# Kernel tuning notes

Hardware: AMD Instinct MI355X
Metric: run time of the kernel (lower is better)

## Reference

```python
import jax, jax.numpy as jnp
import numpy as np

N_EMBD = 1024
N_HEAD = 16

def setup_inputs() -> dict:
    key = jax.random.key(0)
    ks = jax.random.split(key, 5)
    s = 0.02
    return {
        "x": jax.random.normal(ks[0], (4, 2048, N_EMBD), dtype=jnp.float32),
        "w_attn": jax.random.normal(ks[1], (N_EMBD, 3 * N_EMBD), dtype=jnp.float32) * s,
        "b_attn": jnp.zeros((3 * N_EMBD,), dtype=jnp.float32),
        "w_proj": jax.random.normal(ks[2], (N_EMBD, N_EMBD), dtype=jnp.float32) * s,
        "b_proj": jnp.zeros((N_EMBD,), dtype=jnp.float32),
    }

def reference(x, w_attn, b_attn, w_proj, b_proj):
    B, T, C = x.shape
    H = N_HEAD
    D = C // H
    qkv = x @ w_attn + b_attn                       # [B,T,3C]
    q, k, v = jnp.split(qkv, 3, axis=-1)
    # [B,H,T,D]
    q = q.reshape(B, T, H, D).transpose(0, 2, 1, 3)
    k = k.reshape(B, T, H, D).transpose(0, 2, 1, 3)
    v = v.reshape(B, T, H, D).transpose(0, 2, 1, 3)
    scale = 1.0 / jnp.sqrt(jnp.asarray(D, dtype=x.dtype))
    attn = jnp.einsum("bhqd,bhkd->bhqk", q, k) * scale
    mask = jnp.tril(jnp.ones((T, T), dtype=bool))
    attn = jnp.where(mask, attn, jnp.asarray(-jnp.inf, dtype=attn.dtype))
    attn = jax.nn.softmax(attn, axis=-1)
    out = jnp.einsum("bhqk,bhkd->bhqd", attn, v)    # [B,H,T,D]
    out = out.transpose(0, 2, 1, 3).reshape(B, T, C)
    return out @ w_proj + b_proj
```

## Files before the change

### kernel.cpp

```cpp
#include <hip/hip_runtime.h>


typedef unsigned short u16b;
typedef __bf16 bf16x8 __attribute__((ext_vector_type(8)));
typedef float f32x4 __attribute__((ext_vector_type(4)));
typedef float f32x16 __attribute__((ext_vector_type(16)));
typedef unsigned short u16x4 __attribute__((ext_vector_type(4)));

#define AS1(p) ((const __attribute__((address_space(1))) void*)(p))
#define AS3(p) ((__attribute__((address_space(3))) void*)(p))
#define GLDS(g, l) __builtin_amdgcn_global_load_lds(AS1(g), AS3(l), 16, 0, 0)

__device__ __forceinline__ u16b bfr(float v) {
  union { float f; unsigned u; } x; x.f = v;
  unsigned r = x.u + 0x7fffu + ((x.u >> 16) & 1u);
  return (u16b)(r >> 16);
}

__device__ __forceinline__ unsigned pk2(float lo, float hi) {
  union { __bf16 h[2]; unsigned u; } t;
  t.h[0] = (__bf16)lo; t.h[1] = (__bf16)hi;
  return t.u;
}

__global__ __launch_bounds__(256) void cvt_bf16_kernel(
    const float* __restrict__ src, u16b* __restrict__ dst, int n4) {
  int i = blockIdx.x * 256 + threadIdx.x;
  const int stride = gridDim.x * 256;
  for (; i < n4; i += stride) {
    const float4 v = reinterpret_cast<const float4*>(src)[i];
    u16x4 o;
    o[0] = bfr(v.x); o[1] = bfr(v.y); o[2] = bfr(v.z); o[3] = bfr(v.w);
    reinterpret_cast<u16x4*>(dst)[i] = o;
  }
}

__global__ __launch_bounds__(256) void transpose_cvt_kernel(
    const float* __restrict__ src, u16b* __restrict__ dst, int R, int C) {
  __shared__ u16b tile[64][72];
  const int nc = C >> 6;
  const int br = blockIdx.x / nc, bc = blockIdx.x % nc;
  const int r0 = br << 6, c0 = bc << 6;
  const int c = threadIdx.x & 63, r4 = threadIdx.x >> 6;
  #pragma unroll
  for (int i = 0; i < 16; ++i) {
    const int r = r4 + 4 * i;
    tile[r][c] = bfr(src[(size_t)(r0 + r) * C + c0 + c]);
  }
  __syncthreads();
  #pragma unroll
  for (int i = 0; i < 16; ++i) {
    const int rr = r4 + 4 * i;
    dst[(size_t)(c0 + rr) * R + r0 + c] = tile[c][rr];
  }
}

template <int EPI>
__global__ __launch_bounds__(256, 2) void gemm128_kernel(
    const u16b* __restrict__ A, const u16b* __restrict__ Bt,
    const float* __restrict__ bias,
    u16b* __restrict__ oQ, u16b* __restrict__ oK, u16b* __restrict__ oVt,
    float* __restrict__ oF, int M, int N, int K) {
  __shared__ u16b smem[32768];
  const int tid = threadIdx.x;
  const int wid = tid >> 6, lane = tid & 63;
  const int xcd = blockIdx.x & 7;
  const int idx = blockIdx.x >> 3;
  const int stg = idx >> 6, rr6 = idx & 63;
  const int brow = (xcd << 3) + (rr6 >> 3);
  const int bcol = (stg << 3) + (rr6 & 7);
  const int wr = (wid >> 1) << 6, wc = (wid & 1) << 6;

  f32x4 acc[4][4] = {};

  const int srow = (wid << 5) + (lane >> 3);
  const int sc = ((lane & 7) ^ (lane >> 3)) << 3;
  const u16b* Ab = A + (size_t)((brow << 7) + srow) * K + sc;
  const u16b* Bb = Bt + (size_t)((bcol << 7) + srow) * K + sc;
  const int fr = lane & 15;
  const int fq = lane >> 4;
  const int pcs0 = ((fq) ^ (fr & 7)) << 4;
  const int pcs1 = ((4 + fq) ^ (fr & 7)) << 4;
  const int nk = K >> 6;

#define STAGE(bufi, kk)                                                        \
  {                                                                            \
    char* sb = (char*)smem + (bufi) * 32768;                                   \
    _Pragma("unroll")                                                          \
    for (int j = 0; j < 4; ++j)                                                \
      GLDS(Ab + (size_t)8 * K * j + (kk), sb + wid * 4096 + j * 1024);         \
    _Pragma("unroll")                                                          \
    for (int j = 0; j < 4; ++j)                                                \
      GLDS(Bb + (size_t)8 * K * j + (kk), sb + 16384 + wid * 4096 + j * 1024); \
  }

  STAGE(0, 0);
  STAGE(1, 64);

  #pragma unroll 1
  for (int kt = 0; kt < nk; ++kt) {
    if (kt + 1 < nk) asm volatile("s_waitcnt vmcnt(8)" ::: "memory");
    else             asm volatile("s_waitcnt vmcnt(0)" ::: "memory");
    __builtin_amdgcn_s_barrier();

    const char* As = (const char*)smem + (kt & 1) * 32768;
    const char* Bs = As + 16384;
    bf16x8 af0[4], af1[4], bf0[4], bf1[4];
    #pragma unroll
    for (int i = 0; i < 4; ++i) {
      const int rowb = (wr + i * 16 + fr) * 128;
      af0[i] = *(const bf16x8*)(As + rowb + pcs0);
      af1[i] = *(const bf16x8*)(As + rowb + pcs1);
    }
    #pragma unroll
    for (int j = 0; j < 4; ++j) {
      const int rowb = (wc + j * 16 + fr) * 128;
      bf0[j] = *(const bf16x8*)(Bs + rowb + pcs0);
      bf1[j] = *(const bf16x8*)(Bs + rowb + pcs1);
    }
    __builtin_amdgcn_s_setprio(1);
    #pragma unroll
    for (int i = 0; i < 4; ++i)
      #pragma unroll
      for (int j = 0; j < 4; ++j)
        acc[i][j] = __builtin_amdgcn_mfma_f32_16x16x32_bf16(af0[i], bf0[j], acc[i][j], 0, 0, 0);
    #pragma unroll
    for (int i = 0; i < 4; ++i)
      #pragma unroll
      for (int j = 0; j < 4; ++j)
        acc[i][j] = __builtin_amdgcn_mfma_f32_16x16x32_bf16(af1[i], bf1[j], acc[i][j], 0, 0, 0);
    __builtin_amdgcn_s_setprio(0);

    __builtin_amdgcn_s_barrier();
    if (kt + 2 < nk) STAGE(kt & 1, (kt + 2) << 6);
  }
#undef STAGE

  if (EPI == 1) {
    #pragma unroll
    for (int j = 0; j < 4; ++j) {
      const int n0 = (bcol << 7) + wc + j * 16 + fr;
      const float bv = bias[n0];
      #pragma unroll
      for (int i = 0; i < 4; ++i) {
        #pragma unroll
        for (int r = 0; r < 4; ++r) {
          const int m0 = (brow << 7) + wr + i * 16 + fq * 4 + r;
          oF[(size_t)m0 * N + n0] = acc[i][j][r] + bv;
        }
      }
    }
  } else {
    const int sect = bcol >> 3;
    if (sect < 2) {
      const float qs = (sect == 0) ? 0.1803368801f : 1.0f;
      u16b* oPtr = (sect == 0) ? oQ : oK;
      u16b* tile = (u16b*)smem;
      #pragma unroll
      for (int j = 0; j < 4; ++j) {
        const int n = wc + j * 16 + fr;
        const float bv = bias[(bcol << 7) + n];
        #pragma unroll
        for (int i = 0; i < 4; ++i) {
          #pragma unroll
          for (int r = 0; r < 4; ++r) {
            const int m = wr + i * 16 + fq * 4 + r;
            const int byteoff = m * 256 + (((n >> 3) ^ (m & 7)) << 4) + ((n & 7) << 1);
            *(u16b*)((char*)tile + byteoff) = bfr((acc[i][j][r] + bv) * qs);
          }
        }
      }
      __syncthreads();
      const int nh = wid >> 1;
      const int c = lane & 7;
      #pragma unroll
      for (int it = 0; it < 8; ++it) {
        const int m = ((wid & 1) << 6) + (it << 3) + (lane >> 3);
        const int chunk = (nh << 3) + (c ^ (m & 7));
        const bf16x8 val = *(const bf16x8*)((const char*)tile + m * 256 + chunk * 16);
        const int m0 = (brow << 7) + m;
        const int n0 = (bcol << 7) + (nh << 6) + (c << 3);
        const int bb = m0 >> 11, tt = m0 & 2047;
        const int h = (n0 >> 6) & 15, d = n0 & 63;
        *(bf16x8*)(oPtr + (((size_t)(bb * 16 + h) * 2048 + tt) * 64 + d)) = val;
      }
    } else {
      u16b* tile = (u16b*)smem;
      #pragma unroll
      for (int j = 0; j < 4; ++j) {
        const int nl = wc + j * 16 + fr;
        const float bv = bias[(bcol << 7) + nl];
        #pragma unroll
        for (int i = 0; i < 4; ++i) {
          #pragma unroll
          for (int r = 0; r < 4; ++r) {
            const int m = wr + i * 16 + fq * 4 + r;
            const int byteoff = nl * 256 + (((m >> 3) ^ (nl & 7)) << 4) + ((m & 7) << 1);
            *(u16b*)((char*)tile + byteoff) = bfr(acc[i][j][r] + bv);
          }
        }
      }
      __syncthreads();
      const int row0 = wid << 5;
      const int c16 = lane & 15;
      const int rw = lane >> 4;
      const int t0 = (brow << 7) & 2047;
      const int bb = brow >> 4;
      #pragma unroll
      for (int it = 0; it < 8; ++it) {
        const int nl = row0 + (it << 2) + rw;
        const int pch = c16 ^ (nl & 7);
        const bf16x8 val = *(const bf16x8*)((const char*)tile + nl * 256 + pch * 16);
        const int h = ((bcol & 7) << 1) + (nl >> 6);
        const int d = nl & 63;
        *(bf16x8*)(oVt + ((size_t)((bb << 4) + h) * 64 + d) * 2048 + t0 + (c16 << 3)) = val;
      }
    }
  }
}

__global__ __launch_bounds__(256, 3) void flash_kernel(
    const u16b* __restrict__ Q, const u16b* __restrict__ K,
    const u16b* __restrict__ Vt, u16b* __restrict__ O) {
  __shared__ u16b smem[24576];
  const int bid = blockIdx.x;
  const int bh = bid & 63;
  const int qt = 15 - (bid >> 6);
  const int tid = threadIdx.x, wid = tid >> 6, lane = tid & 63;
  const int ln31 = lane & 31, hi = lane >> 5;
  const size_t baseQK = (size_t)bh * 2048 * 64;
  const size_t baseV = (size_t)bh * 64 * 2048;
  const int b = bh >> 4, h = bh & 15;
  const int srow = wid * 8 + (lane >> 3);
  const int sc = ((lane & 7) ^ (srow & 7)) << 3;

  const int q0w = (qt << 7) + wid * 32;
  const int NT = 2 * qt + 2;
  const int LT = q0w >> 6;

#define FSTAGE(kt, bi)                                                         \
  {                                                                            \
    char* kb_ = (char*)smem + (bi) * 16384;                                    \
    const int k0_ = (kt) << 6;                                                 \
    GLDS(K + baseQK + (size_t)(k0_ + srow) * 64 + sc,        kb_ + wid * 1024);\
    GLDS(K + baseQK + (size_t)(k0_ + 32 + srow) * 64 + sc,   kb_ + 4096 + wid * 1024);\
    GLDS(Vt + baseV + (size_t)srow * 2048 + k0_ + sc,        kb_ + 8192 + wid * 1024);\
    GLDS(Vt + baseV + (size_t)(32 + srow) * 2048 + k0_ + sc, kb_ + 12288 + wid * 1024);\
  }

  bf16x8 qf[4];
  {
    const u16b* qp = Q + baseQK + (size_t)(q0w + ln31) * 64 + hi * 8;
    #pragma unroll
    for (int kk = 0; kk < 4; ++kk) qf[kk] = *(const bf16x8*)(qp + kk * 16);
  }
  bf16x8 ones;
  {
    union { u16b s[8]; bf16x8 v; } o1;
    #pragma unroll
    for (int i = 0; i < 8; ++i) o1.s[i] = 0x3F80;
    ones = o1.v;
  }

  f32x16 oa0 = {}, oa1 = {}, lacc = {};

  FSTAGE(0, 0);
  FSTAGE(1, 1);

  int buf = 0;
  int nbuf = 2;
  #pragma unroll 1
  for (int kt = 0; kt < NT; ++kt) {
    if (kt + 1 < NT) asm volatile("s_waitcnt vmcnt(4)" ::: "memory");
    else             asm volatile("s_waitcnt vmcnt(0)" ::: "memory");
    __builtin_amdgcn_s_barrier();

    if (kt + 2 < NT) FSTAGE(kt + 2, nbuf);

    if (kt <= LT) {
      const char* kb = (const char*)smem + buf * 16384;
      const char* vb = kb + 8192;
      const bool diag = (kt == LT);
      const int maxsub = diag ? (wid & 1) : 1;

      f32x16 s[2] = {};
      __builtin_amdgcn_s_setprio(1);
      #pragma unroll
      for (int ss = 0; ss < 2; ++ss) {
        if (ss <= maxsub) {
          const int row = 32 * ss + ln31;
          #pragma unroll
          for (int kk = 0; kk < 4; ++kk) {
            const int ch = (2 * kk + hi) ^ (row & 7);
            const bf16x8 kf = *(const bf16x8*)(kb + row * 128 + ch * 16);
            s[ss] = __builtin_amdgcn_mfma_f32_32x32x16_bf16(kf, qf[kk], s[ss], 0, 0, 0);
          }
        }
      }
      __builtin_amdgcn_s_setprio(0);

      if (diag) {
        #pragma unroll
        for (int ss = 0; ss < 2; ++ss) {
          if (ss == (wid & 1)) {
            #pragma unroll
            for (int r = 0; r < 16; ++r) {
              const int kvr = (r & 3) + 8 * (r >> 2) + 4 * hi;
              if (kvr > ln31) s[ss][r] = -3e38f;
            }
          }
        }
      }

      #pragma unroll
      for (int ss = 0; ss < 2; ++ss) {
        if (ss <= maxsub) {
          #pragma unroll
          for (int r = 0; r < 16; ++r)
            s[ss][r] = __builtin_amdgcn_exp2f(s[ss][r]);
        }
      }

      union WB { unsigned u[4]; bf16x8 v; };
      __builtin_amdgcn_s_setprio(1);
      #pragma unroll
      for (int ss = 0; ss < 2; ++ss) {
        if (ss <= maxsub) {
          WB pA, pB;
#define MKPA(W0, W1, W2, W3, P0, P1, P2, P3, P4, P5, P6, P7)                 \
          {                                                                   \
            unsigned a0 = pk2(P0, P1), a1 = pk2(P2, P3);                      \
            unsigned b0 = pk2(P4, P5), b1 = pk2(P6, P7);                      \
            auto r0 = __builtin_amdgcn_permlane32_swap(a0, b0, false, false); \
            auto r1 = __builtin_amdgcn_permlane32_swap(a1, b1, false, false); \
            unsigned o0[2], o1[2];                                            \
            __builtin_memcpy(o0, &r0, 8); __builtin_memcpy(o1, &r1, 8);       \
            W0 = o0[0]; W2 = o0[1]; W1 = o1[0]; W3 = o1[1];                   \
          }
          MKPA(pA.u[0], pA.u[1], pA.u[2], pA.u[3],
               s[ss][0], s[ss][1], s[ss][2], s[ss][3],
               s[ss][4], s[ss][5], s[ss][6], s[ss][7]);
          MKPA(pB.u[0], pB.u[1], pB.u[2], pB.u[3],
               s[ss][8], s[ss][9], s[ss][10], s[ss][11],
               s[ss][12], s[ss][13], s[ss][14], s[ss][15]);
#undef MKPA
          const int r0v = ln31, r1v = 32 + ln31;
          const char* v0 = vb + r0v * 128;
          const char* v1 = vb + r1v * 128;
          const int chA0 = ((4 * ss + hi) ^ (r0v & 7)) << 4;
          const int chA1 = ((4 * ss + hi) ^ (r1v & 7)) << 4;
          const int chB0 = ((4 * ss + 2 + hi) ^ (r0v & 7)) << 4;
          const int chB1 = ((4 * ss + 2 + hi) ^ (r1v & 7)) << 4;
          lacc = __builtin_amdgcn_mfma_f32_32x32x16_bf16(ones, pA.v, lacc, 0, 0, 0);
          oa0 = __builtin_amdgcn_mfma_f32_32x32x16_bf16(*(const bf16x8*)(v0 + chA0), pA.v, oa0, 0, 0, 0);
          oa1 = __builtin_amdgcn_mfma_f32_32x32x16_bf16(*(const bf16x8*)(v1 + chA1), pA.v, oa1, 0, 0, 0);
          lacc = __builtin_amdgcn_mfma_f32_32x32x16_bf16(ones, pB.v, lacc, 0, 0, 0);
          oa0 = __builtin_amdgcn_mfma_f32_32x32x16_bf16(*(const bf16x8*)(v0 + chB0), pB.v, oa0, 0, 0, 0);
          oa1 = __builtin_amdgcn_mfma_f32_32x32x16_bf16(*(const bf16x8*)(v1 + chB1), pB.v, oa1, 0, 0, 0);
        }
      }
      __builtin_amdgcn_s_setprio(0);
    }

    buf = (buf == 2) ? 0 : buf + 1;
    nbuf = (nbuf == 2) ? 0 : nbuf + 1;
  }

  const float inv = 1.0f / lacc[0];
  const int q = q0w + ln31;
  u16b* orow = O + (size_t)(b * 2048 + q) * 1024 + h * 64;
  #pragma unroll
  for (int rq = 0; rq < 4; ++rq) {
    u16x4 v0, v1;
    #pragma unroll
    for (int j = 0; j < 4; ++j) {
      v0[j] = bfr(oa0[4 * rq + j] * inv);
      v1[j] = bfr(oa1[4 * rq + j] * inv);
    }
    const int d0 = 8 * rq + 4 * hi;
    *(u16x4*)(orow + d0) = v0;
    *(u16x4*)(orow + 32 + d0) = v1;
  }
#undef FSTAGE
}

extern "C" void kernel_launch(void* const* d_in, const int* in_sizes, int n_in,
                              void* d_out, int out_size, void* d_ws, size_t ws_size,
                              hipStream_t stream) {
  const float* x      = (const float*)d_in[0];
  const float* w_attn = (const float*)d_in[1];
  const float* b_attn = (const float*)d_in[2];
  const float* w_proj = (const float*)d_in[3];
  const float* b_proj = (const float*)d_in[4];
  float* out = (float*)d_out;
  char* ws = (char*)d_ws;

  u16b* xb  = (u16b*)(ws + 0);
  u16b* waT = (u16b*)(ws + 16777216);
  u16b* wpT = (u16b*)(ws + 23068672);
  u16b* Qb  = (u16b*)(ws + 25165824);
  u16b* Kb  = (u16b*)(ws + 41943040);
  u16b* Vtb = (u16b*)(ws + 75497472);
  u16b* attn = xb;

  cvt_bf16_kernel<<<2048, 256, 0, stream>>>(x, xb, (8192 * 1024) / 4);
  transpose_cvt_kernel<<<16 * 48, 256, 0, stream>>>(w_attn, waT, 1024, 3072);
  transpose_cvt_kernel<<<16 * 16, 256, 0, stream>>>(w_proj, wpT, 1024, 1024);
  gemm128_kernel<0><<<64 * 24, 256, 0, stream>>>(xb, waT, b_attn, Qb, Kb, Vtb, nullptr,
                                                 8192, 3072, 1024);
  flash_kernel<<<1024, 256, 0, stream>>>(Qb, Kb, Vtb, attn);
  gemm128_kernel<1><<<64 * 8, 256, 0, stream>>>(attn, wpT, b_proj, nullptr, nullptr, nullptr,
                                                out, 8192, 1024, 1024);
}
```

Measured before the change: 150.6 us.

## Switch GEMM to triple-buffered BK=32 pipeline with higher occupancy

```diff
diff --git a/kernel.cpp b/kernel.cpp
--- a/kernel.cpp
+++ b/kernel.cpp
@@ -56,12 +56,12 @@
 }
 
 template <int EPI>
-__global__ __launch_bounds__(256, 2) void gemm128_kernel(
+__global__ __launch_bounds__(256, 3) void gemm128_kernel(
     const u16b* __restrict__ A, const u16b* __restrict__ Bt,
     const float* __restrict__ bias,
     u16b* __restrict__ oQ, u16b* __restrict__ oK, u16b* __restrict__ oVt,
     float* __restrict__ oF, int M, int N, int K) {
-  __shared__ u16b smem[32768];
+  __shared__ u16b smem[24576];
   const int tid = threadIdx.x;
   const int wid = tid >> 6, lane = tid & 63;
   const int xcd = blockIdx.x & 7;
@@ -73,69 +73,61 @@
 
   f32x4 acc[4][4] = {};
 
-  const int srow = (wid << 5) + (lane >> 3);
-  const int sc = ((lane & 7) ^ (lane >> 3)) << 3;
-  const u16b* Ab = A + (size_t)((brow << 7) + srow) * K + sc;
-  const u16b* Bb = Bt + (size_t)((bcol << 7) + srow) * K + sc;
+  const int ar = (wid << 4) + (lane >> 2);
+  const int acs = (((lane & 3) ^ ((lane >> 3) & 3))) << 3;
+  const u16b* Ab = A + (size_t)((brow << 7) + ar) * K + acs;
+  const u16b* Bb = Bt + (size_t)((bcol << 7) + ar) * K + acs;
   const int fr = lane & 15;
   const int fq = lane >> 4;
-  const int pcs0 = ((fq) ^ (fr & 7)) << 4;
-  const int pcs1 = ((4 + fq) ^ (fr & 7)) << 4;
-  const int nk = K >> 6;
-
-#define STAGE(bufi, kk)                                                        \
+  const int pcs = ((fq ^ ((fr >> 1) & 3))) << 4;
+  const int nk = K >> 5;
+
+#define STAGE(t, bi)                                                           \
   {                                                                            \
-    char* sb = (char*)smem + (bufi) * 32768;                                   \
-    _Pragma("unroll")                                                          \
-    for (int j = 0; j < 4; ++j)                                                \
-      GLDS(Ab + (size_t)8 * K * j + (kk), sb + wid * 4096 + j * 1024);         \
-    _Pragma("unroll")                                                          \
-    for (int j = 0; j < 4; ++j)                                                \
-      GLDS(Bb + (size_t)8 * K * j + (kk), sb + 16384 + wid * 4096 + j * 1024); \
+    char* sb = (char*)smem + (bi) * 16384;                                     \
+    GLDS(Ab + (size_t)(t) * 32,                  sb + wid * 1024);             \
+    GLDS(Ab + (size_t)64 * K + (size_t)(t) * 32, sb + 4096 + wid * 1024);      \
+    GLDS(Bb + (size_t)(t) * 32,                  sb + 8192 + wid * 1024);      \
+    GLDS(Bb + (size_t)64 * K + (size_t)(t) * 32, sb + 12288 + wid * 1024);     \
   }
 
   STAGE(0, 0);
-  STAGE(1, 64);
-
+  STAGE(1, 1);
+
+  int buf = 0, nbuf = 2;
   #pragma unroll 1
   for (int kt = 0; kt < nk; ++kt) {
-    if (kt + 1 < nk) asm volatile("s_waitcnt vmcnt(8)" ::: "memory");
+    if (kt + 1 < nk) asm volatile("s_waitcnt vmcnt(4)" ::: "memory");
     else             asm volatile("s_waitcnt vmcnt(0)" ::: "memory");
     __builtin_amdgcn_s_barrier();
 
-    const char* As = (const char*)smem + (kt & 1) * 32768;
-    const char* Bs = As + 16384;
-    bf16x8 af0[4], af1[4], bf0[4], bf1[4];
-    #pragma unroll
-    for (int i = 0; i < 4; ++i) {
-      const int rowb = (wr + i * 16 + fr) * 128;
-      af0[i] = *(const bf16x8*)(As + rowb + pcs0);
-      af1[i] = *(const bf16x8*)(As + rowb + pcs1);
-    }
-    #pragma unroll
-    for (int j = 0; j < 4; ++j) {
-      const int rowb = (wc + j * 16 + fr) * 128;
-      bf0[j] = *(const bf16x8*)(Bs + rowb + pcs0);
-      bf1[j] = *(const bf16x8*)(Bs + rowb + pcs1);
-    }
+    if (kt + 2 < nk) STAGE(kt + 2, nbuf);
+
+    const char* As = (const char*)smem + buf * 16384;
+    const char* Bs = As + 8192;
+    bf16x8 af[4], bfv[4];
+    #pragma unroll
+    for (int i = 0; i < 4; ++i)
+      af[i] = *(const bf16x8*)(As + (wr + i * 16 + fr) * 64 + pcs);
+    #pragma unroll
+    for (int j = 0; j < 4; ++j)
+      bfv[j] = *(const bf16x8*)(Bs + (wc + j * 16 + fr) * 64 + pcs);
     __builtin_amdgcn_s_setprio(1);
     #pragma unroll
     for (int i = 0; i < 4; ++i)
       #pragma unroll
       for (int j = 0; j < 4; ++j)
-        acc[i][j] = __builtin_amdgcn_mfma_f32_16x16x32_bf16(af0[i], bf0[j], acc[i][j], 0, 0, 0);
-    #pragma unroll
-    for (int i = 0; i < 4; ++i)
-      #pragma unroll
-      for (int j = 0; j < 4; ++j)
-        acc[i][j] = __builtin_amdgcn_mfma_f32_16x16x32_bf16(af1[i], bf1[j], acc[i][j], 0, 0, 0);
+        acc[i][j] = __builtin_amdgcn_mfma_f32_16x16x32_bf16(af[i], bfv[j], acc[i][j], 0, 0, 0);
     __builtin_amdgcn_s_setprio(0);
 
-    __builtin_amdgcn_s_barrier();
-    if (kt + 2 < nk) STAGE(kt & 1, (kt + 2) << 6);
+    buf = (buf == 2) ? 0 : buf + 1;
+    nbuf = (nbuf == 2) ? 0 : nbuf + 1;
   }
 #undef STAGE
 
+  __syncthreads();
+
+  const int fq2 = lane >> 4;
   if (EPI == 1) {
     #pragma unroll
     for (int j = 0; j < 4; ++j) {
@@ -145,7 +137,7 @@
       for (int i = 0; i < 4; ++i) {
         #pragma unroll
         for (int r = 0; r < 4; ++r) {
-          const int m0 = (brow << 7) + wr + i * 16 + fq * 4 + r;
+          const int m0 = (brow << 7) + wr + i * 16 + fq2 * 4 + r;
           oF[(size_t)m0 * N + n0] = acc[i][j][r] + bv;
         }
       }
@@ -164,7 +156,7 @@
         for (int i = 0; i < 4; ++i) {
           #pragma unroll
           for (int r = 0; r < 4; ++r) {
-            const int m = wr + i * 16 + fq * 4 + r;
+            const int m = wr + i * 16 + fq2 * 4 + r;
             const int byteoff = m * 256 + (((n >> 3) ^ (m & 7)) << 4) + ((n & 7) << 1);
             *(u16b*)((char*)tile + byteoff) = bfr((acc[i][j][r] + bv) * qs);
           }
@@ -194,7 +186,7 @@
         for (int i = 0; i < 4; ++i) {
           #pragma unroll
           for (int r = 0; r < 4; ++r) {
-            const int m = wr + i * 16 + fq * 4 + r;
+            const int m = wr + i * 16 + fq2 * 4 + r;
             const int byteoff = nl * 256 + (((m >> 3) ^ (nl & 7)) << 4) + ((m & 7) << 1);
             *(u16b*)((char*)tile + byteoff) = bfr(acc[i][j][r] + bv);
           }
```

Result: slower. 156.3 us (+3.8%).

## Pair short and long causal query tiles per flash block to share K/V loads

Applied to the files above, without the earlier changes.

```diff
diff --git a/kernel.cpp b/kernel.cpp
--- a/kernel.cpp
+++ b/kernel.cpp
@@ -219,13 +219,15 @@
   }
 }
 
-__global__ __launch_bounds__(256, 3) void flash_kernel(
+__global__ __launch_bounds__(256, 2) void flash_kernel(
     const u16b* __restrict__ Q, const u16b* __restrict__ K,
     const u16b* __restrict__ Vt, u16b* __restrict__ O) {
   __shared__ u16b smem[24576];
   const int bid = blockIdx.x;
   const int bh = bid & 63;
-  const int qt = 15 - (bid >> 6);
+  const int dp = bid >> 6;
+  const int p = (dp < 4) ? dp : (11 - dp);
+  const int g1 = p, g2 = 15 - p;
   const int tid = threadIdx.x, wid = tid >> 6, lane = tid & 63;
   const int ln31 = lane & 31, hi = lane >> 5;
   const size_t baseQK = (size_t)bh * 2048 * 64;
@@ -234,9 +236,11 @@
   const int srow = wid * 8 + (lane >> 3);
   const int sc = ((lane & 7) ^ (srow & 7)) << 3;
 
-  const int q0w = (qt << 7) + wid * 32;
-  const int NT = 2 * qt + 2;
-  const int LT = q0w >> 6;
+  const int q0wA = (g1 << 7) + wid * 32;
+  const int q0wB = (g2 << 7) + wid * 32;
+  const int LTA = q0wA >> 6;
+  const int LTB = q0wB >> 6;
+  const int NT = 2 * g2 + 2;
 
 #define FSTAGE(kt, bi)                                                         \
   {                                                                            \
@@ -248,11 +252,15 @@
     GLDS(Vt + baseV + (size_t)(32 + srow) * 2048 + k0_ + sc, kb_ + 12288 + wid * 1024);\
   }
 
-  bf16x8 qf[4];
+  bf16x8 qfA[4], qfB[4];
   {
-    const u16b* qp = Q + baseQK + (size_t)(q0w + ln31) * 64 + hi * 8;
-    #pragma unroll
-    for (int kk = 0; kk < 4; ++kk) qf[kk] = *(const bf16x8*)(qp + kk * 16);
+    const u16b* qpA = Q + baseQK + (size_t)(q0wA + ln31) * 64 + hi * 8;
+    const u16b* qpB = Q + baseQK + (size_t)(q0wB + ln31) * 64 + hi * 8;
+    #pragma unroll
+    for (int kk = 0; kk < 4; ++kk) {
+      qfA[kk] = *(const bf16x8*)(qpA + kk * 16);
+      qfB[kk] = *(const bf16x8*)(qpB + kk * 16);
+    }
   }
   bf16x8 ones;
   {
@@ -262,13 +270,13 @@
     ones = o1.v;
   }
 
-  f32x16 oa0 = {}, oa1 = {}, lacc = {};
+  f32x16 oaA0 = {}, oaA1 = {}, laccA = {};
+  f32x16 oaB0 = {}, oaB1 = {}, laccB = {};
 
   FSTAGE(0, 0);
   FSTAGE(1, 1);
 
-  int buf = 0;
-  int nbuf = 2;
+  int buf = 0, nbuf = 2;
   #pragma unroll 1
   for (int kt = 0; kt < NT; ++kt) {
     if (kt + 1 < NT) asm volatile("s_waitcnt vmcnt(4)" ::: "memory");
@@ -277,9 +285,11 @@
 
     if (kt + 2 < NT) FSTAGE(kt + 2, nbuf);
 
-    if (kt <= LT) {
-      const char* kb = (const char*)smem + buf * 16384;
-      const char* vb = kb + 8192;
+    const char* kb = (const char*)smem + buf * 16384;
+    const char* vb = kb + 8192;
+
+    auto compute_tile = [&](const bf16x8* qf, f32x16& oa0, f32x16& oa1,
+                            f32x16& lacc, const int LT) {
       const bool diag = (kt == LT);
       const int maxsub = diag ? (wid & 1) : 1;
 
@@ -360,26 +370,48 @@
         }
       }
       __builtin_amdgcn_s_setprio(0);
-    }
+    };
+
+    if (kt <= LTB) compute_tile(qfB, oaB0, oaB1, laccB, LTB);
+    if (kt <= LTA) compute_tile(qfA, oaA0, oaA1, laccA, LTA);
 
     buf = (buf == 2) ? 0 : buf + 1;
     nbuf = (nbuf == 2) ? 0 : nbuf + 1;
   }
 
-  const float inv = 1.0f / lacc[0];
-  const int q = q0w + ln31;
-  u16b* orow = O + (size_t)(b * 2048 + q) * 1024 + h * 64;
-  #pragma unroll
-  for (int rq = 0; rq < 4; ++rq) {
-    u16x4 v0, v1;
-    #pragma unroll
-    for (int j = 0; j < 4; ++j) {
-      v0[j] = bfr(oa0[4 * rq + j] * inv);
-      v1[j] = bfr(oa1[4 * rq + j] * inv);
-    }
-    const int d0 = 8 * rq + 4 * hi;
-    *(u16x4*)(orow + d0) = v0;
-    *(u16x4*)(orow + 32 + d0) = v1;
+  {
+    const float inv = 1.0f / laccA[0];
+    const int q = q0wA + ln31;
+    u16b* orow = O + (size_t)(b * 2048 + q) * 1024 + h * 64;
+    #pragma unroll
+    for (int rq = 0; rq < 4; ++rq) {
+      u16x4 v0, v1;
+      #pragma unroll
+      for (int j = 0; j < 4; ++j) {
+        v0[j] = bfr(oaA0[4 * rq + j] * inv);
+        v1[j] = bfr(oaA1[4 * rq + j] * inv);
+      }
+      const int d0 = 8 * rq + 4 * hi;
+      *(u16x4*)(orow + d0) = v0;
+      *(u16x4*)(orow + 32 + d0) = v1;
+    }
+  }
+  {
+    const float inv = 1.0f / laccB[0];
+    const int q = q0wB + ln31;
+    u16b* orow = O + (size_t)(b * 2048 + q) * 1024 + h * 64;
+    #pragma unroll
+    for (int rq = 0; rq < 4; ++rq) {
+      u16x4 v0, v1;
+      #pragma unroll
+      for (int j = 0; j < 4; ++j) {
+        v0[j] = bfr(oaB0[4 * rq + j] * inv);
+        v1[j] = bfr(oaB1[4 * rq + j] * inv);
+      }
+      const int d0 = 8 * rq + 4 * hi;
+      *(u16x4*)(orow + d0) = v0;
+      *(u16x4*)(orow + 32 + d0) = v1;
+    }
   }
 #undef FSTAGE
 }
@@ -408,7 +440,7 @@
   transpose_cvt_kernel<<<16 * 16, 256, 0, stream>>>(w_proj, wpT, 1024, 1024);
   gemm128_kernel<0><<<64 * 24, 256, 0, stream>>>(xb, waT, b_attn, Qb, Kb, Vtb, nullptr,
                                                  8192, 3072, 1024);
-  flash_kernel<<<1024, 256, 0, stream>>>(Qb, Kb, Vtb, attn);
+  flash_kernel<<<512, 256, 0, stream>>>(Qb, Kb, Vtb, attn);
   gemm128_kernel<1><<<64 * 8, 256, 0, stream>>>(attn, wpT, b_proj, nullptr, nullptr, nullptr,
                                                 out, 8192, 1024, 1024);
 }
```

Result: no change. 152.2 us (+1.1%).
